# Kernel optimization log

Hardware: AMD Instinct MI355X
Metric: run time of the kernel (lower is better)

## Reference

```python
import jax, jax.numpy as jnp
import numpy as np

IN_G, OUT_G, IN_MEM, OUT_MEM, N_EMBED = 64, 64, 8, 8, 512
DIM_QUANT = IN_MEM * OUT_MEM  # 64
B = 8192


def setup_inputs() -> dict:
    key = jax.random.key(0)
    k1, k2, k3 = jax.random.split(key, 3)
    x = jax.random.normal(k1, (B, IN_G * IN_MEM), dtype=jnp.float32)
    # xavier-uniform-ish init for weight
    bound = float(np.sqrt(6.0 / (IN_MEM + OUT_MEM)))
    weight = jax.random.uniform(k2, (IN_G, OUT_G, IN_MEM, OUT_MEM), dtype=jnp.float32,
                                minval=-bound, maxval=bound)
    # VQ codebook, stored (dim, n_embed) as in rosinality Quantize
    embed = jax.random.normal(k3, (DIM_QUANT, N_EMBED), dtype=jnp.float32)
    return {"x": x, "weight": weight, "embed": embed, "use_qw": 1}


def _quantize(w_flat, embed):
    # w_flat: [G, dim]; embed: [dim, n_embed]
    # dist = ||w||^2 - 2 w@e + ||e||^2  (squared euclidean)
    dist = ((w_flat ** 2).sum(axis=1, keepdims=True)
            - 2.0 * (w_flat @ embed)
            + (embed ** 2).sum(axis=0, keepdims=True))
    idx = jnp.argmin(dist, axis=1)
    quant = jnp.take(embed.T, idx, axis=0)  # embed_code: embedding on embed.T
    return quant, idx


def reference(x, weight, embed, use_qw):
    in_g, out_g, in_mem, out_mem = weight.shape
    b = x.shape[0]
    xg = x.reshape(b, in_g, in_mem).transpose(1, 0, 2)  # [g, b, i]
    if use_qw:
        w_flat = weight.reshape(in_g * out_g, in_mem * out_mem)
        quant, _ = _quantize(w_flat, embed)
        quant = quant.reshape(weight.shape)
        diff = jnp.mean((jax.lax.stop_gradient(quant) - weight) ** 2)
        # straight-through estimator
        q_w = weight + jax.lax.stop_gradient(quant - weight)
    else:
        q_w = weight
        diff = None
    # permute(0,2,1,3).reshape -> [g, in_mem, out_g*out_mem]
    q_w = q_w.transpose(0, 2, 1, 3).reshape(in_g, in_mem, out_g * out_mem)
    # grouped matmul + stack + sum over groups == single einsum contraction over g and i
    res = jnp.einsum('gbi,gio->bo', xg, q_w)  # [b, out_g*out_mem]
    return (res, diff)
```

## Files before the change

### kernel.cpp

```cpp
#include <hip/hip_runtime.h>
#include <cstdint>

#define NEMB   512
#define DQ     64
#define NROWS  4096
#define BATCH  8192
#define KDIM   512
#define NDIM   512

#define CONV_BLOCKS 2048
#define VQ_BLOCKS   256

typedef __attribute__((ext_vector_type(8))) short bf16x8;
typedef __attribute__((ext_vector_type(4))) float floatx4;

__device__ __forceinline__ unsigned short f2bf(float f) {
    unsigned int u = __float_as_uint(f);
    u += 0x7fffu + ((u >> 16) & 1u);
    return (unsigned short)(u >> 16);
}

__device__ __forceinline__ void async16(const void* g, void* l) {
    __builtin_amdgcn_global_load_lds(
        (const __attribute__((address_space(1))) void*)g,
        (__attribute__((address_space(3))) void*)l, 16, 0, 0);
}

__global__ __launch_bounds__(256) void fused_prep_vq(
    const float* __restrict__ x,
    const float* __restrict__ weight,
    const float* __restrict__ embed,
    unsigned short* __restrict__ xb,
    unsigned short* __restrict__ wt,
    float* __restrict__ partials,
    const int* __restrict__ use_qw)
{
    const int t   = threadIdx.x;
    const int bid = blockIdx.x;

    if (bid < CONV_BLOCKS) {
        const int gid = bid * 256 + t;
#pragma unroll
        for (int it = 0; it < 2; ++it) {
            const int idx = gid + it * 524288;
            float4 v = reinterpret_cast<const float4*>(x)[idx];
            ushort4 o;
            o.x = f2bf(v.x); o.y = f2bf(v.y); o.z = f2bf(v.z); o.w = f2bf(v.w);
            reinterpret_cast<ushort4*>(xb)[idx] = o;
        }
        return;
    }

    const int vb   = bid - CONV_BLOCKS;
    const int wave = t >> 6;
    const int lane = t & 63;
    const int rblk = vb * 16;
    const bool qon = (use_qw[0] != 0);

    __shared__ float wlds[16 * 64];
    __shared__ int   bidx_lds[16];
    __shared__ float red[4];

    reinterpret_cast<float4*>(wlds)[t] =
        reinterpret_cast<const float4*>(weight + (size_t)rblk * 64)[t];
    __syncthreads();

    if (qon) {
        const int j0 = lane * 8;
        const int rw = wave * 4;

        double acc[4][8];
        double ee[8];
#pragma unroll
        for (int c = 0; c < 8; ++c) ee[c] = 0.0;
#pragma unroll
        for (int r = 0; r < 4; ++r)
#pragma unroll
            for (int c = 0; c < 8; ++c) acc[r][c] = 0.0;

        for (int d = 0; d < DQ; ++d) {
            const float4 ea = *reinterpret_cast<const float4*>(embed + d * NEMB + j0);
            const float4 eb = *reinterpret_cast<const float4*>(embed + d * NEMB + j0 + 4);
            double ev[8];
            ev[0] = (double)ea.x; ev[1] = (double)ea.y; ev[2] = (double)ea.z; ev[3] = (double)ea.w;
            ev[4] = (double)eb.x; ev[5] = (double)eb.y; ev[6] = (double)eb.z; ev[7] = (double)eb.w;
#pragma unroll
            for (int c = 0; c < 8; ++c) ee[c] = fma(ev[c], ev[c], ee[c]);
#pragma unroll
            for (int r = 0; r < 4; ++r) {
                const double wv = (double)wlds[(rw + r) * 64 + d];
#pragma unroll
                for (int c = 0; c < 8; ++c)
                    acc[r][c] = fma(wv, ev[c], acc[r][c]);
            }
        }

#pragma unroll
        for (int r = 0; r < 4; ++r) {
            double best = 1e300;
            int bi = 0;
#pragma unroll
            for (int c = 0; c < 8; ++c) {
                const double q = fma(-2.0, acc[r][c], ee[c]);
                if (q < best) { best = q; bi = j0 + c; }
            }
#pragma unroll
            for (int off = 1; off < 64; off <<= 1) {
                const double ob = __shfl_xor(best, off, 64);
                const int    oi = __shfl_xor(bi,   off, 64);
                if (ob < best || (ob == best && oi < bi)) { best = ob; bi = oi; }
            }
            if (lane == 0) bidx_lds[rw + r] = bi;
        }
    }
    __syncthreads();

    float dsum = 0.f;
    if (t < 128) {
        const int rloc = t >> 3, om = t & 7;
        const int row = rblk + rloc;
        const int g = row >> 6, og = row & 63;
        const int bidx = qon ? bidx_lds[rloc] : 0;
        alignas(16) unsigned short q8[8];
#pragma unroll
        for (int i = 0; i < 8; ++i) {
            const int d = i * 8 + om;
            const float wv = wlds[rloc * 64 + d];
            float qv;
            if (qon) {
                qv = embed[d * NEMB + bidx];
                const float df = qv - wv;
                dsum = fmaf(df, df, dsum);
            } else {
                qv = wv;
            }
            q8[i] = f2bf(qv);
        }
        *reinterpret_cast<int4*>(wt + (size_t)(og * 8 + om) * KDIM + g * 8) =
            *reinterpret_cast<const int4*>(q8);
    }

#pragma unroll
    for (int off = 32; off > 0; off >>= 1) dsum += __shfl_down(dsum, off, 64);
    if (lane == 0) red[wave] = dsum;
    __syncthreads();
    if (t == 0) partials[vb] = red[0] + red[1] + red[2] + red[3];
}

__global__ __launch_bounds__(256, 4) void gemm_kernel(
    const unsigned short* __restrict__ xb,
    const unsigned short* __restrict__ wt,
    float* __restrict__ out,
    const float* __restrict__ partials,
    float* diff_slot)
{
    __shared__ unsigned short As[64 * 32];
    __shared__ unsigned short Bs[64 * 32];

    const int tid  = threadIdx.x;
    const int wave = tid >> 6;
    const int lane = tid & 63;

    const int flat = blockIdx.x;
    const int xcd  = flat & 7;
    const int idx  = flat >> 3;
    const int mt   = xcd * 16 + (idx >> 3);
    const int nt   = idx & 7;
    const int m0 = mt * 64;
    const int n0 = nt * 64;
    const int wm = (wave >> 1) * 32;
    const int wn = (wave & 1) * 32;

    const int srow = lane >> 2;
    const int scol = (lane & 3) * 8;
    const int mrow = lane & 15;
    const int koff = (lane >> 4) * 8;

    floatx4 acc[2][2] = {};

    for (int k0 = 0; k0 < KDIM; k0 += 32) {
        __syncthreads();
        {
            const int row = wave * 16 + srow;
            async16(xb + (size_t)(m0 + row) * KDIM + k0 + scol, (char*)As + wave * 1024);
            async16(wt + (size_t)(n0 + row) * KDIM + k0 + scol, (char*)Bs + wave * 1024);
        }
        __syncthreads();

        bf16x8 a[2], b[2];
#pragma unroll
        for (int i = 0; i < 2; ++i)
            a[i] = *reinterpret_cast<const bf16x8*>(&As[(wm + i * 16 + mrow) * 32 + koff]);
#pragma unroll
        for (int j = 0; j < 2; ++j)
            b[j] = *reinterpret_cast<const bf16x8*>(&Bs[(wn + j * 16 + mrow) * 32 + koff]);
#pragma unroll
        for (int i = 0; i < 2; ++i)
#pragma unroll
            for (int j = 0; j < 2; ++j)
                acc[i][j] = __builtin_amdgcn_mfma_f32_16x16x32_bf16(a[i], b[j], acc[i][j], 0, 0, 0);
    }

    const int col = lane & 15;
    const int rbase = (lane >> 4) * 4;
#pragma unroll
    for (int i = 0; i < 2; ++i)
#pragma unroll
        for (int j = 0; j < 2; ++j)
#pragma unroll
            for (int r = 0; r < 4; ++r) {
                const int mm = m0 + wm + i * 16 + rbase + r;
                const int nn = n0 + wn + j * 16 + col;
                out[(size_t)mm * NDIM + nn] = acc[i][j][r];
            }

    if (flat == 0 && wave == 0 && diff_slot) {
        float s = partials[lane] + partials[lane + 64]
                + partials[lane + 128] + partials[lane + 192];
#pragma unroll
        for (int off = 32; off > 0; off >>= 1) s += __shfl_down(s, off, 64);
        if (lane == 0) diff_slot[0] = s * (1.f / (NROWS * DQ));
    }
}

extern "C" void kernel_launch(void* const* d_in, const int* in_sizes, int n_in,
                              void* d_out, int out_size, void* d_ws, size_t ws_size,
                              hipStream_t stream)
{
    const float* x      = (const float*)d_in[0];
    const float* weight = (const float*)d_in[1];
    const float* embed  = (const float*)d_in[2];
    const int*   use_qw = (const int*)d_in[3];
    float* out = (float*)d_out;

    unsigned short* wt   = (unsigned short*)d_ws;
    float* partials      = (float*)((char*)d_ws + (512u << 10));
    unsigned short* xb   = (unsigned short*)((char*)d_ws + (1u << 20));

    float* diff_slot = (out_size > BATCH * NDIM) ? (out + (size_t)BATCH * NDIM) : nullptr;

    fused_prep_vq<<<CONV_BLOCKS + VQ_BLOCKS, 256, 0, stream>>>(
        x, weight, embed, xb, wt, partials, use_qw);
    gemm_kernel<<<1024, 256, 0, stream>>>(xb, wt, out, partials, diff_slot);
}
```

Baseline: 122.1 us.

## Enlarge GEMM tiles with swizzled LDS and rebalance VQ blocks first

The GEMM tile grows from 64x64x32 to 128x64x64, with an XOR-swizzled LDS layout to avoid bank conflicts, which halves the grid and gives each wave twice as many MFMAs per load. The VQ part now runs 512 blocks of 8 rows, placed ahead of the conversion blocks so the heavier double-precision work is scheduled first. Codebook norms are precomputed once per block into LDS rather than accumulated inside the distance loop. The costs are fewer GEMM blocks (lower occupancy and parallelism) and redundant norm computation in every VQ block.

Result: faster. 100.0 us (-18.1%).

```diff
diff --git a/kernel.cpp b/kernel.cpp
--- a/kernel.cpp
+++ b/kernel.cpp
@@ -8,8 +8,8 @@
 #define KDIM   512
 #define NDIM   512
 
+#define VQ_BLOCKS   512
 #define CONV_BLOCKS 2048
-#define VQ_BLOCKS   256
 
 typedef __attribute__((ext_vector_type(8))) short bf16x8;
 typedef __attribute__((ext_vector_type(4))) float floatx4;
@@ -38,8 +38,8 @@
     const int t   = threadIdx.x;
     const int bid = blockIdx.x;
 
-    if (bid < CONV_BLOCKS) {
-        const int gid = bid * 256 + t;
+    if (bid >= VQ_BLOCKS) {
+        const int gid = (bid - VQ_BLOCKS) * 256 + t;
 #pragma unroll
         for (int it = 0; it < 2; ++it) {
             const int idx = gid + it * 524288;
@@ -51,32 +51,38 @@
         return;
     }
 
-    const int vb   = bid - CONV_BLOCKS;
     const int wave = t >> 6;
     const int lane = t & 63;
-    const int rblk = vb * 16;
+    const int rblk = bid * 8;
     const bool qon = (use_qw[0] != 0);
 
-    __shared__ float wlds[16 * 64];
-    __shared__ int   bidx_lds[16];
-    __shared__ float red[4];
-
-    reinterpret_cast<float4*>(wlds)[t] =
-        reinterpret_cast<const float4*>(weight + (size_t)rblk * 64)[t];
+    __shared__ float  wlds[8 * 64];
+    __shared__ double e2lds[NEMB];
+    __shared__ int    bidx_lds[8];
+
+    if (t < 128)
+        reinterpret_cast<float4*>(wlds)[t] =
+            reinterpret_cast<const float4*>(weight + (size_t)rblk * 64)[t];
+
+    {
+        double s0 = 0.0, s1 = 0.0;
+        for (int d = 0; d < DQ; ++d) {
+            const float2 e = *reinterpret_cast<const float2*>(embed + d * NEMB + 2 * t);
+            s0 = fma((double)e.x, (double)e.x, s0);
+            s1 = fma((double)e.y, (double)e.y, s1);
+        }
+        e2lds[2 * t]     = s0;
+        e2lds[2 * t + 1] = s1;
+    }
     __syncthreads();
 
     if (qon) {
         const int j0 = lane * 8;
-        const int rw = wave * 4;
-
-        double acc[4][8];
-        double ee[8];
-#pragma unroll
-        for (int c = 0; c < 8; ++c) ee[c] = 0.0;
-#pragma unroll
-        for (int r = 0; r < 4; ++r)
-#pragma unroll
-            for (int c = 0; c < 8; ++c) acc[r][c] = 0.0;
+        const int r0 = wave * 2;
+
+        double a0[8], a1[8];
+#pragma unroll
+        for (int c = 0; c < 8; ++c) { a0[c] = 0.0; a1[c] = 0.0; }
 
         for (int d = 0; d < DQ; ++d) {
             const float4 ea = *reinterpret_cast<const float4*>(embed + d * NEMB + j0);
@@ -84,24 +90,21 @@
             double ev[8];
             ev[0] = (double)ea.x; ev[1] = (double)ea.y; ev[2] = (double)ea.z; ev[3] = (double)ea.w;
             ev[4] = (double)eb.x; ev[5] = (double)eb.y; ev[6] = (double)eb.z; ev[7] = (double)eb.w;
-#pragma unroll
-            for (int c = 0; c < 8; ++c) ee[c] = fma(ev[c], ev[c], ee[c]);
-#pragma unroll
-            for (int r = 0; r < 4; ++r) {
-                const double wv = (double)wlds[(rw + r) * 64 + d];
-#pragma unroll
-                for (int c = 0; c < 8; ++c)
-                    acc[r][c] = fma(wv, ev[c], acc[r][c]);
-            }
-        }
-
-#pragma unroll
-        for (int r = 0; r < 4; ++r) {
+            const double w0 = (double)wlds[r0 * 64 + d];
+            const double w1 = (double)wlds[r0 * 64 + 64 + d];
+#pragma unroll
+            for (int c = 0; c < 8; ++c) a0[c] = fma(w0, ev[c], a0[c]);
+#pragma unroll
+            for (int c = 0; c < 8; ++c) a1[c] = fma(w1, ev[c], a1[c]);
+        }
+
+#pragma unroll
+        for (int r = 0; r < 2; ++r) {
             double best = 1e300;
             int bi = 0;
 #pragma unroll
             for (int c = 0; c < 8; ++c) {
-                const double q = fma(-2.0, acc[r][c], ee[c]);
+                const double q = fma(-2.0, (r == 0 ? a0[c] : a1[c]), e2lds[j0 + c]);
                 if (q < best) { best = q; bi = j0 + c; }
             }
 #pragma unroll
@@ -110,13 +113,13 @@
                 const int    oi = __shfl_xor(bi,   off, 64);
                 if (ob < best || (ob == best && oi < bi)) { best = ob; bi = oi; }
             }
-            if (lane == 0) bidx_lds[rw + r] = bi;
+            if (lane == 0) bidx_lds[r0 + r] = bi;
         }
     }
     __syncthreads();
 
     float dsum = 0.f;
-    if (t < 128) {
+    if (t < 64) {
         const int rloc = t >> 3, om = t & 7;
         const int row = rblk + rloc;
         const int g = row >> 6, og = row & 63;
@@ -139,23 +142,22 @@
         *reinterpret_cast<int4*>(wt + (size_t)(og * 8 + om) * KDIM + g * 8) =
             *reinterpret_cast<const int4*>(q8);
     }
-
-#pragma unroll
-    for (int off = 32; off > 0; off >>= 1) dsum += __shfl_down(dsum, off, 64);
-    if (lane == 0) red[wave] = dsum;
-    __syncthreads();
-    if (t == 0) partials[vb] = red[0] + red[1] + red[2] + red[3];
-}
-
-__global__ __launch_bounds__(256, 4) void gemm_kernel(
+    if (wave == 0) {
+#pragma unroll
+        for (int off = 32; off > 0; off >>= 1) dsum += __shfl_down(dsum, off, 64);
+        if (lane == 0) partials[bid] = dsum;
+    }
+}
+
+__global__ __launch_bounds__(256) void gemm_kernel(
     const unsigned short* __restrict__ xb,
     const unsigned short* __restrict__ wt,
     float* __restrict__ out,
     const float* __restrict__ partials,
     float* diff_slot)
 {
-    __shared__ unsigned short As[64 * 32];
-    __shared__ unsigned short Bs[64 * 32];
+    __shared__ unsigned short As[128 * 64];
+    __shared__ unsigned short Bs[64 * 64];
 
     const int tid  = threadIdx.x;
     const int wave = tid >> 6;
@@ -163,48 +165,64 @@
 
     const int flat = blockIdx.x;
     const int xcd  = flat & 7;
-    const int idx  = flat >> 3;
-    const int mt   = xcd * 16 + (idx >> 3);
-    const int nt   = idx & 7;
-    const int m0 = mt * 64;
+    const int sub  = flat >> 3;
+    const int nt   = sub & 7;
+    const int mt   = xcd * 8 + (sub >> 3);
+    const int m0 = mt * 128;
     const int n0 = nt * 64;
-    const int wm = (wave >> 1) * 32;
+    const int wm = (wave >> 1) * 64;
     const int wn = (wave & 1) * 32;
 
-    const int srow = lane >> 2;
-    const int scol = (lane & 3) * 8;
+    const int srow   = lane >> 3;
+    const int schunk = (lane & 7) ^ srow;
     const int mrow = lane & 15;
-    const int koff = (lane >> 4) * 8;
-
-    floatx4 acc[2][2] = {};
-
-    for (int k0 = 0; k0 < KDIM; k0 += 32) {
+    const int cq   = lane >> 4;
+
+    floatx4 acc[4][2] = {};
+
+    for (int k0 = 0; k0 < KDIM; k0 += 64) {
         __syncthreads();
-        {
-            const int row = wave * 16 + srow;
-            async16(xb + (size_t)(m0 + row) * KDIM + k0 + scol, (char*)As + wave * 1024);
-            async16(wt + (size_t)(n0 + row) * KDIM + k0 + scol, (char*)Bs + wave * 1024);
+#pragma unroll
+        for (int c = 0; c < 4; ++c) {
+            const int g = wave * 4 + c;
+            const int row = g * 8 + srow;
+            async16(xb + (size_t)(m0 + row) * KDIM + k0 + schunk * 8, (char*)As + g * 1024);
+        }
+#pragma unroll
+        for (int c = 0; c < 2; ++c) {
+            const int g = wave * 2 + c;
+            const int row = g * 8 + srow;
+            async16(wt + (size_t)(n0 + row) * KDIM + k0 + schunk * 8, (char*)Bs + g * 1024);
         }
         __syncthreads();
 
-        bf16x8 a[2], b[2];
-#pragma unroll
-        for (int i = 0; i < 2; ++i)
-            a[i] = *reinterpret_cast<const bf16x8*>(&As[(wm + i * 16 + mrow) * 32 + koff]);
-#pragma unroll
-        for (int j = 0; j < 2; ++j)
-            b[j] = *reinterpret_cast<const bf16x8*>(&Bs[(wn + j * 16 + mrow) * 32 + koff]);
-#pragma unroll
-        for (int i = 0; i < 2; ++i)
-#pragma unroll
-            for (int j = 0; j < 2; ++j)
-                acc[i][j] = __builtin_amdgcn_mfma_f32_16x16x32_bf16(a[i], b[j], acc[i][j], 0, 0, 0);
+#pragma unroll
+        for (int ks = 0; ks < 2; ++ks) {
+            bf16x8 a[4], b[2];
+#pragma unroll
+            for (int i = 0; i < 4; ++i) {
+                const int r = wm + i * 16 + mrow;
+                const int c = ks * 4 + cq;
+                a[i] = *reinterpret_cast<const bf16x8*>(&As[r * 64 + ((c ^ (r & 7)) * 8)]);
+            }
+#pragma unroll
+            for (int j = 0; j < 2; ++j) {
+                const int r = wn + j * 16 + mrow;
+                const int c = ks * 4 + cq;
+                b[j] = *reinterpret_cast<const bf16x8*>(&Bs[r * 64 + ((c ^ (r & 7)) * 8)]);
+            }
+#pragma unroll
+            for (int i = 0; i < 4; ++i)
+#pragma unroll
+                for (int j = 0; j < 2; ++j)
+                    acc[i][j] = __builtin_amdgcn_mfma_f32_16x16x32_bf16(a[i], b[j], acc[i][j], 0, 0, 0);
+        }
     }
 
     const int col = lane & 15;
     const int rbase = (lane >> 4) * 4;
 #pragma unroll
-    for (int i = 0; i < 2; ++i)
+    for (int i = 0; i < 4; ++i)
 #pragma unroll
         for (int j = 0; j < 2; ++j)
 #pragma unroll
@@ -215,8 +233,9 @@
             }
 
     if (flat == 0 && wave == 0 && diff_slot) {
-        float s = partials[lane] + partials[lane + 64]
-                + partials[lane + 128] + partials[lane + 192];
+        float s = 0.f;
+#pragma unroll
+        for (int q = 0; q < 8; ++q) s += partials[lane + 64 * q];
 #pragma unroll
         for (int off = 32; off > 0; off >>= 1) s += __shfl_down(s, off, 64);
         if (lane == 0) diff_slot[0] = s * (1.f / (NROWS * DQ));
@@ -233,13 +252,13 @@
     const int*   use_qw = (const int*)d_in[3];
     float* out = (float*)d_out;
 
-    unsigned short* wt   = (unsigned short*)d_ws;
-    float* partials      = (float*)((char*)d_ws + (512u << 10));
-    unsigned short* xb   = (unsigned short*)((char*)d_ws + (1u << 20));
+    unsigned short* wt = (unsigned short*)d_ws;
+    float* partials    = (float*)((char*)d_ws + (512u << 10));
+    unsigned short* xb = (unsigned short*)((char*)d_ws + (1u << 20));
 
     float* diff_slot = (out_size > BATCH * NDIM) ? (out + (size_t)BATCH * NDIM) : nullptr;
 
-    fused_prep_vq<<<CONV_BLOCKS + VQ_BLOCKS, 256, 0, stream>>>(
+    fused_prep_vq<<<VQ_BLOCKS + CONV_BLOCKS, 256, 0, stream>>>(
         x, weight, embed, xb, wt, partials, use_qw);
-    gemm_kernel<<<1024, 256, 0, stream>>>(xb, wt, out, partials, diff_slot);
-}
+    gemm_kernel<<<512, 256, 0, stream>>>(xb, wt, out, partials, diff_slot);
+}
```
